# Kernel tuning notes

Measured on AMD Instinct MI355X. Metric: run time of the kernel, lower is better.

Reference implementation:

```python
import jax, jax.numpy as jnp
import numpy as np

B, S, D, H = 2, 2048, 1024, 16
DK = D // H

def setup_inputs() -> dict:
    key = jax.random.key(0)
    ks = jax.random.split(key, 12)
    def lin(k, shape, fan_in):
        bound = 1.0 / np.sqrt(fan_in)
        return jax.random.uniform(k, shape, jnp.float32, -bound, bound)
    inp = {
        'Q': jax.random.normal(ks[0], (B, S, D), jnp.float32),
        'K': jax.random.normal(ks[1], (B, S, D), jnp.float32),
        'V': jax.random.normal(ks[2], (B, S, D), jnp.float32),
        # padding mask: last 128 key positions of batch element 0 are padding
        'padding_mask': jnp.ones((B, 1, 1, S), jnp.int32).at[0, :, :, -128:].set(0),
        # causal look-ahead mask
        'look_ahead_mask': jnp.tril(jnp.ones((S, S), jnp.int32))[None, None],
        'Wq': lin(ks[3], (D, D), D), 'bq': lin(ks[4], (D,), D),
        'Wk': lin(ks[5], (D, D), D), 'bk': lin(ks[6], (D,), D),
        'Wv': lin(ks[7], (D, D), D), 'bv': lin(ks[8], (D,), D),
        'Wo': lin(ks[9], (D, D), D), 'bo': lin(ks[10], (D,), D),
    }
    return inp

def _split_heads(x):
    # [B,S,D] -> [B,H,S,DK]
    b, s, _ = x.shape
    return x.reshape(b, s, H, DK).transpose(0, 2, 1, 3)

def reference(Q, K, V, padding_mask, look_ahead_mask, Wq, bq, Wk, bk, Wv, bv, Wo, bo):
    q = _split_heads(Q @ Wq.T + bq)  # [B,H,S,DK]
    k = _split_heads(K @ Wk.T + bk)
    v = _split_heads(V @ Wv.T + bv)
    scores = jnp.einsum('bhqd,bhkd->bhqk', q, k) / np.sqrt(DK).astype(np.float32)
    neg_inf = jnp.float32(-jnp.inf)
    scores = jnp.where(padding_mask == 0, neg_inf, scores)
    scores = jnp.where(look_ahead_mask == 0, neg_inf, scores)
    weights = jax.nn.softmax(scores, axis=-1)  # dropout is identity in eval mode
    x = jnp.einsum('bhqk,bhkd->bhqd', weights, v)  # [B,H,S,DK]
    x = x.transpose(0, 2, 1, 3).reshape(Q.shape[0], Q.shape[1], D)
    return x @ Wo.T + bo
```

## Files before the change

### kernel.cpp

```cpp
#include <hip/hip_runtime.h>
#include <hip/hip_bf16.h>

#define B_   2
#define S_   2048
#define D_   1024
#define H_   16
#define DK_  64

typedef unsigned short u16;
typedef __attribute__((ext_vector_type(8))) short bf16x8;
typedef __attribute__((ext_vector_type(4))) float f32x4;

static __device__ __forceinline__ u16 f2bf(float f) {
  union { float f; unsigned u; } v; v.f = f;
  unsigned r = v.u + 0x7FFF + ((v.u >> 16) & 1);
  return (u16)(r >> 16);
}

static __device__ __forceinline__ void gl_lds16(const void* g, void* l) {
  __builtin_amdgcn_global_load_lds(
      (const __attribute__((address_space(1))) void*)g,
      (__attribute__((address_space(3))) void*)l, 16, 0, 0);
}

__global__ void cvt3(const float4* __restrict__ a, const float4* __restrict__ b, const float4* __restrict__ c,
                     ushort4* __restrict__ oa, ushort4* __restrict__ ob, ushort4* __restrict__ oc, int n4) {
  int y = blockIdx.y;
  const float4* in = (y == 0) ? a : (y == 1) ? b : c;
  ushort4* out = (y == 0) ? oa : (y == 1) ? ob : oc;
  int i = blockIdx.x * blockDim.x + threadIdx.x;
  if (i < n4) {
    float4 v = in[i];
    ushort4 r;
    r.x = f2bf(v.x); r.y = f2bf(v.y); r.z = f2bf(v.z); r.w = f2bf(v.w);
    out[i] = r;
  }
}
__global__ void cvt4(const float4* __restrict__ a, const float4* __restrict__ b, const float4* __restrict__ c,
                     const float4* __restrict__ d, ushort4* __restrict__ oa, ushort4* __restrict__ ob,
                     ushort4* __restrict__ oc, ushort4* __restrict__ od, int n4) {
  int y = blockIdx.y;
  const float4* in = (y == 0) ? a : (y == 1) ? b : (y == 2) ? c : d;
  ushort4* out = (y == 0) ? oa : (y == 1) ? ob : (y == 2) ? oc : od;
  int i = blockIdx.x * blockDim.x + threadIdx.x;
  if (i < n4) {
    float4 v = in[i];
    ushort4 r;
    r.x = f2bf(v.x); r.y = f2bf(v.y); r.z = f2bf(v.z); r.w = f2bf(v.w);
    out[i] = r;
  }
}

__launch_bounds__(256, 2)
__global__ void gemm_qkv(const u16* __restrict__ Xq, const u16* __restrict__ Xk, const u16* __restrict__ Xv,
                         const u16* __restrict__ Wq, const u16* __restrict__ Wk, const u16* __restrict__ Wv,
                         const float* __restrict__ bq, const float* __restrict__ bk, const float* __restrict__ bv,
                         u16* __restrict__ outq, u16* __restrict__ outk, u16* __restrict__ outv) {
  const int z = blockIdx.z;
  const u16* Am; const u16* Bm; int m0, n0;
  if (z == 2) { Am = Wv; Bm = Xv; m0 = blockIdx.x * 128; n0 = blockIdx.y * 128; }
  else if (z == 1) { Am = Xk; Bm = Wk; m0 = blockIdx.y * 128; n0 = blockIdx.x * 128; }
  else { Am = Xq; Bm = Wq; m0 = blockIdx.y * 128; n0 = blockIdx.x * 128; }
  const float* bias = (z == 0) ? bq : (z == 1) ? bk : bv;

  __shared__ __align__(16) u16 As[128 * 32];
  __shared__ __align__(16) u16 Bs[128 * 32];

  const int tid = threadIdx.x, lane = tid & 63, w = tid >> 6;
  const int q = lane >> 4, cl = lane & 15;
  const int wr = w >> 1, wc = w & 1;

  f32x4 acc[4][4] = {};

  for (int k0 = 0; k0 < D_; k0 += 32) {
#pragma unroll
    for (int i = 0; i < 2; ++i) {
      int cb = (i * 4 + w) * 64;
      int ch = cb + lane;
      int row = ch >> 2, ko = (ch & 3) << 3;
      gl_lds16(Am + (size_t)(m0 + row) * D_ + k0 + ko, As + cb * 8);
      gl_lds16(Bm + (size_t)(n0 + row) * D_ + k0 + ko, Bs + cb * 8);
    }
    __syncthreads();

    bf16x8 af[4], bfr[4];
#pragma unroll
    for (int r = 0; r < 4; ++r) af[r]  = *(const bf16x8*)(As + (wr * 64 + r * 16 + cl) * 32 + q * 8);
#pragma unroll
    for (int c = 0; c < 4; ++c) bfr[c] = *(const bf16x8*)(Bs + (wc * 64 + c * 16 + cl) * 32 + q * 8);
#pragma unroll
    for (int r = 0; r < 4; ++r)
#pragma unroll
      for (int c = 0; c < 4; ++c)
        acc[r][c] = __builtin_amdgcn_mfma_f32_16x16x32_bf16(af[r], bfr[c], acc[r][c], 0, 0, 0);
    __syncthreads();
  }

  if (z == 2) {
#pragma unroll
    for (int r = 0; r < 4; ++r) {
#pragma unroll
      for (int rr = 0; rr < 4; ++rr) {
        int j = m0 + wr * 64 + r * 16 + q * 4 + rr;
        float bval = bias[j];
        int hh = j >> 6, dk = j & 63;
#pragma unroll
        for (int c = 0; c < 4; ++c) {
          int n = n0 + wc * 64 + c * 16 + cl;
          int bb = n >> 11, s = n & (S_ - 1);
          outv[((size_t)(bb * H_ + hh) * DK_ + dk) * S_ + s] = f2bf(acc[r][c][rr] + bval);
        }
      }
    }
  } else {
    const float scale = (z == 0) ? 0.125f : 1.0f;
    u16* o = (z == 0) ? outq : outk;
#pragma unroll
    for (int c = 0; c < 4; ++c) {
      int j = n0 + wc * 64 + c * 16 + cl;
      float bval = bias[j];
      int hh = j >> 6, dk = j & 63;
#pragma unroll
      for (int r = 0; r < 4; ++r) {
#pragma unroll
        for (int rr = 0; rr < 4; ++rr) {
          int n = m0 + wr * 64 + r * 16 + q * 4 + rr;
          int bb = n >> 11, s = n & (S_ - 1);
          o[((size_t)(bb * H_ + hh) * S_ + s) * DK_ + dk] = f2bf((acc[r][c][rr] + bval) * scale);
        }
      }
    }
  }
}

__launch_bounds__(256, 2)
__global__ void attn(const u16* __restrict__ qh, const u16* __restrict__ kh,
                     const u16* __restrict__ vt, const int* __restrict__ pad,
                     u16* __restrict__ attn_out) {
  __shared__ __align__(16) u16 Ks[64 * 64];
  __shared__ __align__(16) u16 Vs[64 * 64];
  __shared__ __align__(16) u16 Ps[4][16 * 72];
  __shared__ float Kbias[64];

  const int tid = threadIdx.x, lane = tid & 63, w = tid >> 6;
  const int q = lane >> 4, cl = lane & 15;
  const int qt = (int)gridDim.x - 1 - (int)blockIdx.x;
  const int qb = qt * 64, h = blockIdx.y, b = blockIdx.z;

  const u16* Q = qh + (size_t)(b * H_ + h) * S_ * DK_;
  const u16* K = kh + (size_t)(b * H_ + h) * S_ * DK_;
  const u16* V = vt + (size_t)(b * H_ + h) * DK_ * S_;
  const int* pm = pad + b * S_;

  const int qr0 = qb + w * 16;
  bf16x8 qf0 = *(const bf16x8*)(Q + (qr0 + cl) * DK_ + q * 8);
  bf16x8 qf1 = *(const bf16x8*)(Q + (qr0 + cl) * DK_ + 32 + q * 8);

  f32x4 o[4] = {};
  float ls[4] = {0.f, 0.f, 0.f, 0.f};
  u16* Pw = Ps[w];

  const int nkv = qt + 1;
  for (int it = 0; it < nkv; ++it) {
    const int kb = it << 6;
#pragma unroll
    for (int i = 0; i < 2; ++i) {
      int s = (i * 4 + w) * 64 + lane;
      int row = s >> 3;
      int c = (s & 7) ^ (row & 7);
      gl_lds16(K + (size_t)(kb + row) * DK_ + (c << 3), Ks + (size_t)s * 8);
      gl_lds16(V + (size_t)row * S_ + kb + (c << 3), Vs + (size_t)s * 8);
    }
    if (tid < 64) {
      Kbias[tid] = (pm[kb + tid] != 0) ? -6.0f : -3e38f;
    }
    __syncthreads();

    f32x4 sa[4];
#pragma unroll
    for (int ct = 0; ct < 4; ++ct) {
      int rk = ct * 16 + cl;
      int c0 = q ^ (rk & 7);
      bf16x8 kf0 = *(const bf16x8*)(Ks + rk * 64 + (c0 << 3));
      bf16x8 kf1 = *(const bf16x8*)(Ks + rk * 64 + ((c0 ^ 4) << 3));
      f32x4 zz = {};
      zz = __builtin_amdgcn_mfma_f32_16x16x32_bf16(qf0, kf0, zz, 0, 0, 0);
      zz = __builtin_amdgcn_mfma_f32_16x16x32_bf16(qf1, kf1, zz, 0, 0, 0);
      sa[ct] = zz;
    }

    if (it < qt) {
#pragma unroll
      for (int ct = 0; ct < 4; ++ct) {
        float kbv = Kbias[ct * 16 + cl];
#pragma unroll
        for (int rr = 0; rr < 4; ++rr) {
          float p = __expf(sa[ct][rr] + kbv);
          ls[rr] += p;
          Pw[(q * 4 + rr) * 72 + ct * 16 + cl] = f2bf(p);
        }
      }
    } else {
#pragma unroll
      for (int ct = 0; ct < 4; ++ct) {
        int kg = kb + ct * 16 + cl;
        float kbv = Kbias[ct * 16 + cl];
#pragma unroll
        for (int rr = 0; rr < 4; ++rr) {
          int qg = qr0 + q * 4 + rr;
          float p = (kg <= qg) ? __expf(sa[ct][rr] + kbv) : 0.f;
          ls[rr] += p;
          Pw[(q * 4 + rr) * 72 + ct * 16 + cl] = f2bf(p);
        }
      }
    }

    bf16x8 pf0 = *(const bf16x8*)(Pw + cl * 72 + q * 8);
    bf16x8 pf1 = *(const bf16x8*)(Pw + cl * 72 + 32 + q * 8);

#pragma unroll
    for (int ct = 0; ct < 4; ++ct) {
      int rv = ct * 16 + cl;
      int c0 = q ^ (rv & 7);
      bf16x8 vf0 = *(const bf16x8*)(Vs + rv * 64 + (c0 << 3));
      bf16x8 vf1 = *(const bf16x8*)(Vs + rv * 64 + ((c0 ^ 4) << 3));
      o[ct] = __builtin_amdgcn_mfma_f32_16x16x32_bf16(pf0, vf0, o[ct], 0, 0, 0);
      o[ct] = __builtin_amdgcn_mfma_f32_16x16x32_bf16(pf1, vf1, o[ct], 0, 0, 0);
    }
    __syncthreads();
  }

#pragma unroll
  for (int rr = 0; rr < 4; ++rr) {
    float l = ls[rr];
    l += __shfl_xor(l, 1, 64);
    l += __shfl_xor(l, 2, 64);
    l += __shfl_xor(l, 4, 64);
    l += __shfl_xor(l, 8, 64);
    float inv = 1.0f / l;
    int qg = qr0 + q * 4 + rr;
    size_t base = (size_t)(b * S_ + qg) * D_ + h * DK_;
#pragma unroll
    for (int ct = 0; ct < 4; ++ct)
      attn_out[base + ct * 16 + cl] = f2bf(o[ct][rr] * inv);
  }
}

__launch_bounds__(256, 2)
__global__ void gemm_out(const u16* __restrict__ A, const u16* __restrict__ W,
                         const float* __restrict__ bias, float* __restrict__ out) {
  __shared__ __align__(16) u16 As[128 * 32];
  __shared__ __align__(16) u16 Bs[128 * 32];

  const int tid = threadIdx.x, lane = tid & 63, w = tid >> 6;
  const int q = lane >> 4, cl = lane & 15;
  const int wr = w >> 1, wc = w & 1;
  const int m0 = blockIdx.y * 128, n0 = blockIdx.x * 128;

  f32x4 acc[4][4] = {};

  for (int k0 = 0; k0 < D_; k0 += 32) {
#pragma unroll
    for (int i = 0; i < 2; ++i) {
      int cb = (i * 4 + w) * 64;
      int ch = cb + lane;
      int row = ch >> 2, ko = (ch & 3) << 3;
      gl_lds16(A + (size_t)(m0 + row) * D_ + k0 + ko, As + cb * 8);
      gl_lds16(W + (size_t)(n0 + row) * D_ + k0 + ko, Bs + cb * 8);
    }
    __syncthreads();

    bf16x8 af[4], bfr[4];
#pragma unroll
    for (int r = 0; r < 4; ++r) af[r]  = *(const bf16x8*)(As + (wr * 64 + r * 16 + cl) * 32 + q * 8);
#pragma unroll
    for (int c = 0; c < 4; ++c) bfr[c] = *(const bf16x8*)(Bs + (wc * 64 + c * 16 + cl) * 32 + q * 8);
#pragma unroll
    for (int r = 0; r < 4; ++r)
#pragma unroll
      for (int c = 0; c < 4; ++c)
        acc[r][c] = __builtin_amdgcn_mfma_f32_16x16x32_bf16(af[r], bfr[c], acc[r][c], 0, 0, 0);
    __syncthreads();
  }

#pragma unroll
  for (int c = 0; c < 4; ++c) {
    int j = n0 + wc * 64 + c * 16 + cl;
    float bval = bias[j];
#pragma unroll
    for (int r = 0; r < 4; ++r) {
#pragma unroll
      for (int rr = 0; rr < 4; ++rr) {
        int n = m0 + wr * 64 + r * 16 + q * 4 + rr;
        out[(size_t)n * D_ + j] = acc[r][c][rr] + bval;
      }
    }
  }
}

extern "C" void kernel_launch(void* const* d_in, const int* in_sizes, int n_in,
                              void* d_out, int out_size, void* d_ws, size_t ws_size,
                              hipStream_t stream) {
  const float* Qf  = (const float*)d_in[0];
  const float* Kf  = (const float*)d_in[1];
  const float* Vf  = (const float*)d_in[2];
  const int*   pad = (const int*)d_in[3];
  const float* Wqf = (const float*)d_in[5];
  const float* bq  = (const float*)d_in[6];
  const float* Wkf = (const float*)d_in[7];
  const float* bk  = (const float*)d_in[8];
  const float* Wvf = (const float*)d_in[9];
  const float* bv  = (const float*)d_in[10];
  const float* Wof = (const float*)d_in[11];
  const float* bo  = (const float*)d_in[12];

  const size_t BSD = (size_t)B_ * S_ * D_;
  const size_t DD  = (size_t)D_ * D_;

  char* ws = (char*)d_ws;
  u16* Qb   = (u16*)ws; ws += BSD * 2;
  u16* Kb   = (u16*)ws; ws += BSD * 2;
  u16* Vb   = (u16*)ws; ws += BSD * 2;
  u16* Wqb  = (u16*)ws; ws += DD * 2;
  u16* Wkb  = (u16*)ws; ws += DD * 2;
  u16* Wvb  = (u16*)ws; ws += DD * 2;
  u16* Wob  = (u16*)ws; ws += DD * 2;
  u16* qhd  = (u16*)ws; ws += BSD * 2;
  u16* khd  = (u16*)ws; ws += BSD * 2;
  u16* vtd  = (u16*)ws; ws += BSD * 2;
  u16* attn_o = (u16*)ws; ws += BSD * 2;

  const int n4 = (int)(BSD / 4);
  const int w4 = (int)(DD / 4);
  dim3 gc3(n4 / 256, 3), gc4(w4 / 256, 4);
  cvt3<<<gc3, 256, 0, stream>>>((const float4*)Qf, (const float4*)Kf, (const float4*)Vf,
                                (ushort4*)Qb, (ushort4*)Kb, (ushort4*)Vb, n4);
  cvt4<<<gc4, 256, 0, stream>>>((const float4*)Wqf, (const float4*)Wkf, (const float4*)Wvf, (const float4*)Wof,
                                (ushort4*)Wqb, (ushort4*)Wkb, (ushort4*)Wvb, (ushort4*)Wob, w4);

  dim3 g1(D_ / 128, (B_ * S_) / 128, 3);
  gemm_qkv<<<g1, 256, 0, stream>>>(Qb, Kb, Vb, Wqb, Wkb, Wvb, bq, bk, bv, qhd, khd, vtd);

  dim3 g2(S_ / 64, H_, B_);
  attn<<<g2, 256, 0, stream>>>(qhd, khd, vtd, pad, attn_o);

  dim3 g3(D_ / 128, (B_ * S_) / 128);
  gemm_out<<<g3, 256, 0, stream>>>(attn_o, Wob, bo, (float*)d_out);
}
```

Baseline: 257.2 us.

## Double-buffer K/V tiles and process 128 query rows per attention block

The attention kernel now handles 128 query rows per block (32 per wave, two MFMA row fragments), so each K/V tile loaded into LDS is reused across twice as many queries. K/V tiles are double-buffered: the next tile is prefetched while the current one is computed, which removes one barrier per iteration. The padding bias is read straight from global memory instead of through an LDS array. The query scale is folded to include log2(e) so exp2f replaces __expf, and the launch bound is raised to 3 blocks per SM. Register pressure rises and the grid shrinks by half, which may hurt occupancy or load balance across the causal triangle.

```diff
diff --git a/kernel.cpp b/kernel.cpp
--- a/kernel.cpp
+++ b/kernel.cpp
@@ -10,6 +10,9 @@
 typedef unsigned short u16;
 typedef __attribute__((ext_vector_type(8))) short bf16x8;
 typedef __attribute__((ext_vector_type(4))) float f32x4;
+
+#define QSCALE   0.18033688011112042f
+#define SMBIAS  -8.656170245333781f
 
 static __device__ __forceinline__ u16 f2bf(float f) {
   union { float f; unsigned u; } v; v.f = f;
@@ -113,7 +116,7 @@
       }
     }
   } else {
-    const float scale = (z == 0) ? 0.125f : 1.0f;
+    const float scale = (z == 0) ? QSCALE : 1.0f;
     u16* o = (z == 0) ? outq : outk;
 #pragma unroll
     for (int c = 0; c < 4; ++c) {
@@ -133,117 +136,158 @@
   }
 }
 
-__launch_bounds__(256, 2)
+__launch_bounds__(256, 3)
 __global__ void attn(const u16* __restrict__ qh, const u16* __restrict__ kh,
                      const u16* __restrict__ vt, const int* __restrict__ pad,
                      u16* __restrict__ attn_out) {
-  __shared__ __align__(16) u16 Ks[64 * 64];
-  __shared__ __align__(16) u16 Vs[64 * 64];
-  __shared__ __align__(16) u16 Ps[4][16 * 72];
-  __shared__ float Kbias[64];
+  __shared__ __align__(16) u16 Ks[2][64 * 64];
+  __shared__ __align__(16) u16 Vs[2][64 * 64];
+  __shared__ __align__(16) u16 Ps[4][32 * 72];
 
   const int tid = threadIdx.x, lane = tid & 63, w = tid >> 6;
   const int q = lane >> 4, cl = lane & 15;
   const int qt = (int)gridDim.x - 1 - (int)blockIdx.x;
-  const int qb = qt * 64, h = blockIdx.y, b = blockIdx.z;
+  const int qb = qt * 128, h = blockIdx.y, b = blockIdx.z;
 
   const u16* Q = qh + (size_t)(b * H_ + h) * S_ * DK_;
   const u16* K = kh + (size_t)(b * H_ + h) * S_ * DK_;
   const u16* V = vt + (size_t)(b * H_ + h) * DK_ * S_;
   const int* pm = pad + b * S_;
 
-  const int qr0 = qb + w * 16;
-  bf16x8 qf0 = *(const bf16x8*)(Q + (qr0 + cl) * DK_ + q * 8);
-  bf16x8 qf1 = *(const bf16x8*)(Q + (qr0 + cl) * DK_ + 32 + q * 8);
-
-  f32x4 o[4] = {};
-  float ls[4] = {0.f, 0.f, 0.f, 0.f};
+  const int qr0 = qb + w * 32;
+  bf16x8 qf[2][2];
+#pragma unroll
+  for (int f = 0; f < 2; ++f) {
+    qf[f][0] = *(const bf16x8*)(Q + (qr0 + f * 16 + cl) * DK_ + q * 8);
+    qf[f][1] = *(const bf16x8*)(Q + (qr0 + f * 16 + cl) * DK_ + 32 + q * 8);
+  }
+
+  f32x4 o[2][4] = {};
+  float ls[2][4] = {};
   u16* Pw = Ps[w];
 
-  const int nkv = qt + 1;
+  const int nkv = 2 * qt + 2;
+
+#pragma unroll
+  for (int i = 0; i < 2; ++i) {
+    int s = (i * 4 + w) * 64 + lane;
+    int row = s >> 3;
+    int c = (s & 7) ^ (row & 7);
+    gl_lds16(K + (size_t)row * DK_ + (c << 3), Ks[0] + (size_t)s * 8);
+    gl_lds16(V + (size_t)row * S_ + (c << 3), Vs[0] + (size_t)s * 8);
+  }
+
   for (int it = 0; it < nkv; ++it) {
     const int kb = it << 6;
-#pragma unroll
-    for (int i = 0; i < 2; ++i) {
-      int s = (i * 4 + w) * 64 + lane;
-      int row = s >> 3;
-      int c = (s & 7) ^ (row & 7);
-      gl_lds16(K + (size_t)(kb + row) * DK_ + (c << 3), Ks + (size_t)s * 8);
-      gl_lds16(V + (size_t)row * S_ + kb + (c << 3), Vs + (size_t)s * 8);
-    }
-    if (tid < 64) {
-      Kbias[tid] = (pm[kb + tid] != 0) ? -6.0f : -3e38f;
-    }
-    __syncthreads();
-
-    f32x4 sa[4];
+    const int buf = it & 1;
+    __syncthreads();
+
+    if (it + 1 < nkv) {
+      const int kb2 = (it + 1) << 6;
+#pragma unroll
+      for (int i = 0; i < 2; ++i) {
+        int s = (i * 4 + w) * 64 + lane;
+        int row = s >> 3;
+        int c = (s & 7) ^ (row & 7);
+        gl_lds16(K + (size_t)(kb2 + row) * DK_ + (c << 3), Ks[buf ^ 1] + (size_t)s * 8);
+        gl_lds16(V + (size_t)row * S_ + kb2 + (c << 3), Vs[buf ^ 1] + (size_t)s * 8);
+      }
+    }
+
+    if (kb > qr0 + 31) continue;
+
+    const u16* Kt = Ks[buf];
+    const u16* Vt = Vs[buf];
+
+    bf16x8 kf[4][2];
 #pragma unroll
     for (int ct = 0; ct < 4; ++ct) {
       int rk = ct * 16 + cl;
       int c0 = q ^ (rk & 7);
-      bf16x8 kf0 = *(const bf16x8*)(Ks + rk * 64 + (c0 << 3));
-      bf16x8 kf1 = *(const bf16x8*)(Ks + rk * 64 + ((c0 ^ 4) << 3));
-      f32x4 zz = {};
-      zz = __builtin_amdgcn_mfma_f32_16x16x32_bf16(qf0, kf0, zz, 0, 0, 0);
-      zz = __builtin_amdgcn_mfma_f32_16x16x32_bf16(qf1, kf1, zz, 0, 0, 0);
-      sa[ct] = zz;
-    }
-
-    if (it < qt) {
+      kf[ct][0] = *(const bf16x8*)(Kt + rk * 64 + (c0 << 3));
+      kf[ct][1] = *(const bf16x8*)(Kt + rk * 64 + ((c0 ^ 4) << 3));
+    }
+
+    float kbv[4];
+#pragma unroll
+    for (int ct = 0; ct < 4; ++ct)
+      kbv[ct] = (pm[kb + ct * 16 + cl] != 0) ? SMBIAS : -3e38f;
+
+    f32x4 sa[2][4];
+#pragma unroll
+    for (int f = 0; f < 2; ++f)
 #pragma unroll
       for (int ct = 0; ct < 4; ++ct) {
-        float kbv = Kbias[ct * 16 + cl];
-#pragma unroll
-        for (int rr = 0; rr < 4; ++rr) {
-          float p = __expf(sa[ct][rr] + kbv);
-          ls[rr] += p;
-          Pw[(q * 4 + rr) * 72 + ct * 16 + cl] = f2bf(p);
+        f32x4 zz = {};
+        zz = __builtin_amdgcn_mfma_f32_16x16x32_bf16(qf[f][0], kf[ct][0], zz, 0, 0, 0);
+        zz = __builtin_amdgcn_mfma_f32_16x16x32_bf16(qf[f][1], kf[ct][1], zz, 0, 0, 0);
+        sa[f][ct] = zz;
+      }
+
+    const bool needmask = (kb + 63 > qr0);
+    if (!needmask) {
+#pragma unroll
+      for (int f = 0; f < 2; ++f)
+#pragma unroll
+        for (int ct = 0; ct < 4; ++ct)
+#pragma unroll
+          for (int rr = 0; rr < 4; ++rr) {
+            float p = exp2f(sa[f][ct][rr] + kbv[ct]);
+            ls[f][rr] += p;
+            Pw[(f * 16 + q * 4 + rr) * 72 + ct * 16 + cl] = f2bf(p);
+          }
+    } else {
+#pragma unroll
+      for (int f = 0; f < 2; ++f)
+#pragma unroll
+        for (int ct = 0; ct < 4; ++ct) {
+          int kg = kb + ct * 16 + cl;
+#pragma unroll
+          for (int rr = 0; rr < 4; ++rr) {
+            int qg = qr0 + f * 16 + q * 4 + rr;
+            float p = (kg <= qg) ? exp2f(sa[f][ct][rr] + kbv[ct]) : 0.f;
+            ls[f][rr] += p;
+            Pw[(f * 16 + q * 4 + rr) * 72 + ct * 16 + cl] = f2bf(p);
+          }
         }
-      }
-    } else {
-#pragma unroll
-      for (int ct = 0; ct < 4; ++ct) {
-        int kg = kb + ct * 16 + cl;
-        float kbv = Kbias[ct * 16 + cl];
-#pragma unroll
-        for (int rr = 0; rr < 4; ++rr) {
-          int qg = qr0 + q * 4 + rr;
-          float p = (kg <= qg) ? __expf(sa[ct][rr] + kbv) : 0.f;
-          ls[rr] += p;
-          Pw[(q * 4 + rr) * 72 + ct * 16 + cl] = f2bf(p);
-        }
-      }
-    }
-
-    bf16x8 pf0 = *(const bf16x8*)(Pw + cl * 72 + q * 8);
-    bf16x8 pf1 = *(const bf16x8*)(Pw + cl * 72 + 32 + q * 8);
-
+    }
+
+    bf16x8 vf[4][2];
 #pragma unroll
     for (int ct = 0; ct < 4; ++ct) {
       int rv = ct * 16 + cl;
       int c0 = q ^ (rv & 7);
-      bf16x8 vf0 = *(const bf16x8*)(Vs + rv * 64 + (c0 << 3));
-      bf16x8 vf1 = *(const bf16x8*)(Vs + rv * 64 + ((c0 ^ 4) << 3));
-      o[ct] = __builtin_amdgcn_mfma_f32_16x16x32_bf16(pf0, vf0, o[ct], 0, 0, 0);
-      o[ct] = __builtin_amdgcn_mfma_f32_16x16x32_bf16(pf1, vf1, o[ct], 0, 0, 0);
-    }
-    __syncthreads();
-  }
-
-#pragma unroll
-  for (int rr = 0; rr < 4; ++rr) {
-    float l = ls[rr];
-    l += __shfl_xor(l, 1, 64);
-    l += __shfl_xor(l, 2, 64);
-    l += __shfl_xor(l, 4, 64);
-    l += __shfl_xor(l, 8, 64);
-    float inv = 1.0f / l;
-    int qg = qr0 + q * 4 + rr;
-    size_t base = (size_t)(b * S_ + qg) * D_ + h * DK_;
-#pragma unroll
-    for (int ct = 0; ct < 4; ++ct)
-      attn_out[base + ct * 16 + cl] = f2bf(o[ct][rr] * inv);
-  }
+      vf[ct][0] = *(const bf16x8*)(Vt + rv * 64 + (c0 << 3));
+      vf[ct][1] = *(const bf16x8*)(Vt + rv * 64 + ((c0 ^ 4) << 3));
+    }
+#pragma unroll
+    for (int f = 0; f < 2; ++f) {
+      bf16x8 pf0 = *(const bf16x8*)(Pw + (f * 16 + cl) * 72 + q * 8);
+      bf16x8 pf1 = *(const bf16x8*)(Pw + (f * 16 + cl) * 72 + 32 + q * 8);
+#pragma unroll
+      for (int ct = 0; ct < 4; ++ct) {
+        o[f][ct] = __builtin_amdgcn_mfma_f32_16x16x32_bf16(pf0, vf[ct][0], o[f][ct], 0, 0, 0);
+        o[f][ct] = __builtin_amdgcn_mfma_f32_16x16x32_bf16(pf1, vf[ct][1], o[f][ct], 0, 0, 0);
+      }
+    }
+  }
+
+#pragma unroll
+  for (int f = 0; f < 2; ++f)
+#pragma unroll
+    for (int rr = 0; rr < 4; ++rr) {
+      float l = ls[f][rr];
+      l += __shfl_xor(l, 1, 64);
+      l += __shfl_xor(l, 2, 64);
+      l += __shfl_xor(l, 4, 64);
+      l += __shfl_xor(l, 8, 64);
+      float inv = 1.0f / l;
+      int qg = qr0 + f * 16 + q * 4 + rr;
+      size_t base = (size_t)(b * S_ + qg) * D_ + h * DK_;
+#pragma unroll
+      for (int ct = 0; ct < 4; ++ct)
+        attn_out[base + ct * 16 + cl] = f2bf(o[f][ct][rr] * inv);
+    }
 }
 
 __launch_bounds__(256, 2)
@@ -341,7 +385,7 @@
   dim3 g1(D_ / 128, (B_ * S_) / 128, 3);
   gemm_qkv<<<g1, 256, 0, stream>>>(Qb, Kb, Vb, Wqb, Wkb, Wvb, bq, bk, bv, qhd, khd, vtd);
 
-  dim3 g2(S_ / 64, H_, B_);
+  dim3 g2(S_ / 128, H_, B_);
   attn<<<g2, 256, 0, stream>>>(qhd, khd, vtd, pad, attn_o);
 
   dim3 g3(D_ / 128, (B_ * S_) / 128);
```

Result: slower. 272.5 us (+5.9%).

## Double-buffer LDS tiles in GEMMs and attention, use exp2 softmax, retile output GEMM

Applied to the files above, without the earlier changes.

Adds two-stage LDS double buffering to the QKV GEMM, the attention loop and the output GEMM, so the next tile's global-to-LDS loads overlap compute and one barrier per iteration is removed. Attention folds log2(e) into the Q scale and bias so it can use exp2f, and it reads the padding mask directly per lane instead of staging it through LDS. The output GEMM moves to a 128x64 tile so twice as many blocks launch. The cost is higher LDS use, which may reduce occupancy, and a single barrier per iteration, which relies on correct ordering of the asynchronous LDS loads.

```diff
diff --git a/kernel.cpp b/kernel.cpp
--- a/kernel.cpp
+++ b/kernel.cpp
@@ -10,6 +10,9 @@
 typedef unsigned short u16;
 typedef __attribute__((ext_vector_type(8))) short bf16x8;
 typedef __attribute__((ext_vector_type(4))) float f32x4;
+
+#define QSCALE   0.18033688011112042f
+#define SMBIAS  -8.656170245333781f
 
 static __device__ __forceinline__ u16 f2bf(float f) {
   union { float f; unsigned u; } v; v.f = f;
@@ -63,37 +66,52 @@
   else { Am = Xq; Bm = Wq; m0 = blockIdx.y * 128; n0 = blockIdx.x * 128; }
   const float* bias = (z == 0) ? bq : (z == 1) ? bk : bv;
 
-  __shared__ __align__(16) u16 As[128 * 32];
-  __shared__ __align__(16) u16 Bs[128 * 32];
+  __shared__ __align__(16) u16 As[2][128 * 32];
+  __shared__ __align__(16) u16 Bs[2][128 * 32];
 
   const int tid = threadIdx.x, lane = tid & 63, w = tid >> 6;
   const int q = lane >> 4, cl = lane & 15;
   const int wr = w >> 1, wc = w & 1;
 
+#pragma unroll
+  for (int i = 0; i < 2; ++i) {
+    int cb = (i * 4 + w) * 64;
+    int ch = cb + lane;
+    int row = ch >> 2, ko = (ch & 3) << 3;
+    gl_lds16(Am + (size_t)(m0 + row) * D_ + ko, As[0] + cb * 8);
+    gl_lds16(Bm + (size_t)(n0 + row) * D_ + ko, Bs[0] + cb * 8);
+  }
+
   f32x4 acc[4][4] = {};
 
-  for (int k0 = 0; k0 < D_; k0 += 32) {
-#pragma unroll
-    for (int i = 0; i < 2; ++i) {
-      int cb = (i * 4 + w) * 64;
-      int ch = cb + lane;
-      int row = ch >> 2, ko = (ch & 3) << 3;
-      gl_lds16(Am + (size_t)(m0 + row) * D_ + k0 + ko, As + cb * 8);
-      gl_lds16(Bm + (size_t)(n0 + row) * D_ + k0 + ko, Bs + cb * 8);
-    }
+  for (int it = 0; it < 32; ++it) {
+    const int buf = it & 1;
     __syncthreads();
 
+    if (it < 31) {
+      const int k0 = (it + 1) * 32;
+#pragma unroll
+      for (int i = 0; i < 2; ++i) {
+        int cb = (i * 4 + w) * 64;
+        int ch = cb + lane;
+        int row = ch >> 2, ko = (ch & 3) << 3;
+        gl_lds16(Am + (size_t)(m0 + row) * D_ + k0 + ko, As[buf ^ 1] + cb * 8);
+        gl_lds16(Bm + (size_t)(n0 + row) * D_ + k0 + ko, Bs[buf ^ 1] + cb * 8);
+      }
+    }
+
+    const u16* At = As[buf];
+    const u16* Bt = Bs[buf];
     bf16x8 af[4], bfr[4];
 #pragma unroll
-    for (int r = 0; r < 4; ++r) af[r]  = *(const bf16x8*)(As + (wr * 64 + r * 16 + cl) * 32 + q * 8);
-#pragma unroll
-    for (int c = 0; c < 4; ++c) bfr[c] = *(const bf16x8*)(Bs + (wc * 64 + c * 16 + cl) * 32 + q * 8);
+    for (int r = 0; r < 4; ++r) af[r]  = *(const bf16x8*)(At + (wr * 64 + r * 16 + cl) * 32 + q * 8);
+#pragma unroll
+    for (int c = 0; c < 4; ++c) bfr[c] = *(const bf16x8*)(Bt + (wc * 64 + c * 16 + cl) * 32 + q * 8);
 #pragma unroll
     for (int r = 0; r < 4; ++r)
 #pragma unroll
       for (int c = 0; c < 4; ++c)
         acc[r][c] = __builtin_amdgcn_mfma_f32_16x16x32_bf16(af[r], bfr[c], acc[r][c], 0, 0, 0);
-    __syncthreads();
   }
 
   if (z == 2) {
@@ -113,7 +131,7 @@
       }
     }
   } else {
-    const float scale = (z == 0) ? 0.125f : 1.0f;
+    const float scale = (z == 0) ? QSCALE : 1.0f;
     u16* o = (z == 0) ? outq : outk;
 #pragma unroll
     for (int c = 0; c < 4; ++c) {
@@ -137,10 +155,9 @@
 __global__ void attn(const u16* __restrict__ qh, const u16* __restrict__ kh,
                      const u16* __restrict__ vt, const int* __restrict__ pad,
                      u16* __restrict__ attn_out) {
-  __shared__ __align__(16) u16 Ks[64 * 64];
-  __shared__ __align__(16) u16 Vs[64 * 64];
+  __shared__ __align__(16) u16 Ks[2][64 * 64];
+  __shared__ __align__(16) u16 Vs[2][64 * 64];
   __shared__ __align__(16) u16 Ps[4][16 * 72];
-  __shared__ float Kbias[64];
 
   const int tid = threadIdx.x, lane = tid & 63, w = tid >> 6;
   const int q = lane >> 4, cl = lane & 15;
@@ -161,54 +178,76 @@
   u16* Pw = Ps[w];
 
   const int nkv = qt + 1;
+
+#pragma unroll
+  for (int i = 0; i < 2; ++i) {
+    int s = (i * 4 + w) * 64 + lane;
+    int row = s >> 3;
+    int c = (s & 7) ^ (row & 7);
+    gl_lds16(K + (size_t)row * DK_ + (c << 3), Ks[0] + (size_t)s * 8);
+    gl_lds16(V + (size_t)row * S_ + (c << 3), Vs[0] + (size_t)s * 8);
+  }
+
   for (int it = 0; it < nkv; ++it) {
     const int kb = it << 6;
-#pragma unroll
-    for (int i = 0; i < 2; ++i) {
-      int s = (i * 4 + w) * 64 + lane;
-      int row = s >> 3;
-      int c = (s & 7) ^ (row & 7);
-      gl_lds16(K + (size_t)(kb + row) * DK_ + (c << 3), Ks + (size_t)s * 8);
-      gl_lds16(V + (size_t)row * S_ + kb + (c << 3), Vs + (size_t)s * 8);
-    }
-    if (tid < 64) {
-      Kbias[tid] = (pm[kb + tid] != 0) ? -6.0f : -3e38f;
-    }
+    const int buf = it & 1;
     __syncthreads();
 
-    f32x4 sa[4];
+    if (it + 1 < nkv) {
+      const int kb2 = (it + 1) << 6;
+#pragma unroll
+      for (int i = 0; i < 2; ++i) {
+        int s = (i * 4 + w) * 64 + lane;
+        int row = s >> 3;
+        int c = (s & 7) ^ (row & 7);
+        gl_lds16(K + (size_t)(kb2 + row) * DK_ + (c << 3), Ks[buf ^ 1] + (size_t)s * 8);
+        gl_lds16(V + (size_t)row * S_ + kb2 + (c << 3), Vs[buf ^ 1] + (size_t)s * 8);
+      }
+    }
+
+    const u16* Kt = Ks[buf];
+    const u16* Vt = Vs[buf];
+
+    bf16x8 kf[4][2];
 #pragma unroll
     for (int ct = 0; ct < 4; ++ct) {
       int rk = ct * 16 + cl;
       int c0 = q ^ (rk & 7);
-      bf16x8 kf0 = *(const bf16x8*)(Ks + rk * 64 + (c0 << 3));
-      bf16x8 kf1 = *(const bf16x8*)(Ks + rk * 64 + ((c0 ^ 4) << 3));
+      kf[ct][0] = *(const bf16x8*)(Kt + rk * 64 + (c0 << 3));
+      kf[ct][1] = *(const bf16x8*)(Kt + rk * 64 + ((c0 ^ 4) << 3));
+    }
+
+    float kbv[4];
+#pragma unroll
+    for (int ct = 0; ct < 4; ++ct)
+      kbv[ct] = (pm[kb + ct * 16 + cl] != 0) ? SMBIAS : -3e38f;
+
+    f32x4 sa[4];
+#pragma unroll
+    for (int ct = 0; ct < 4; ++ct) {
       f32x4 zz = {};
-      zz = __builtin_amdgcn_mfma_f32_16x16x32_bf16(qf0, kf0, zz, 0, 0, 0);
-      zz = __builtin_amdgcn_mfma_f32_16x16x32_bf16(qf1, kf1, zz, 0, 0, 0);
+      zz = __builtin_amdgcn_mfma_f32_16x16x32_bf16(qf0, kf[ct][0], zz, 0, 0, 0);
+      zz = __builtin_amdgcn_mfma_f32_16x16x32_bf16(qf1, kf[ct][1], zz, 0, 0, 0);
       sa[ct] = zz;
     }
 
     if (it < qt) {
 #pragma unroll
-      for (int ct = 0; ct < 4; ++ct) {
-        float kbv = Kbias[ct * 16 + cl];
+      for (int ct = 0; ct < 4; ++ct)
 #pragma unroll
         for (int rr = 0; rr < 4; ++rr) {
-          float p = __expf(sa[ct][rr] + kbv);
+          float p = exp2f(sa[ct][rr] + kbv[ct]);
           ls[rr] += p;
           Pw[(q * 4 + rr) * 72 + ct * 16 + cl] = f2bf(p);
         }
-      }
     } else {
 #pragma unroll
       for (int ct = 0; ct < 4; ++ct) {
         int kg = kb + ct * 16 + cl;
-        float kbv = Kbias[ct * 16 + cl];
 #pragma unroll
         for (int rr = 0; rr < 4; ++rr) {
           int qg = qr0 + q * 4 + rr;
-          float p = (kg <= qg) ? __expf(sa[ct][rr] + kbv) : 0.f;
+          float p = (kg <= qg) ? exp2f(sa[ct][rr] + kbv[ct]) : 0.f;
           ls[rr] += p;
           Pw[(q * 4 + rr) * 72 + ct * 16 + cl] = f2bf(p);
         }
@@ -222,12 +261,11 @@
     for (int ct = 0; ct < 4; ++ct) {
       int rv = ct * 16 + cl;
       int c0 = q ^ (rv & 7);
-      bf16x8 vf0 = *(const bf16x8*)(Vs + rv * 64 + (c0 << 3));
-      bf16x8 vf1 = *(const bf16x8*)(Vs + rv * 64 + ((c0 ^ 4) << 3));
+      bf16x8 vf0 = *(const bf16x8*)(Vt + rv * 64 + (c0 << 3));
+      bf16x8 vf1 = *(const bf16x8*)(Vt + rv * 64 + ((c0 ^ 4) << 3));
       o[ct] = __builtin_amdgcn_mfma_f32_16x16x32_bf16(pf0, vf0, o[ct], 0, 0, 0);
       o[ct] = __builtin_amdgcn_mfma_f32_16x16x32_bf16(pf1, vf1, o[ct], 0, 0, 0);
     }
-    __syncthreads();
   }
 
 #pragma unroll
@@ -249,49 +287,73 @@
 __launch_bounds__(256, 2)
 __global__ void gemm_out(const u16* __restrict__ A, const u16* __restrict__ W,
                          const float* __restrict__ bias, float* __restrict__ out) {
-  __shared__ __align__(16) u16 As[128 * 32];
-  __shared__ __align__(16) u16 Bs[128 * 32];
+  __shared__ __align__(16) u16 As[2][128 * 32];
+  __shared__ __align__(16) u16 Bs[2][64 * 32];
 
   const int tid = threadIdx.x, lane = tid & 63, w = tid >> 6;
   const int q = lane >> 4, cl = lane & 15;
-  const int wr = w >> 1, wc = w & 1;
-  const int m0 = blockIdx.y * 128, n0 = blockIdx.x * 128;
-
-  f32x4 acc[4][4] = {};
-
-  for (int k0 = 0; k0 < D_; k0 += 32) {
-#pragma unroll
-    for (int i = 0; i < 2; ++i) {
-      int cb = (i * 4 + w) * 64;
-      int ch = cb + lane;
-      int row = ch >> 2, ko = (ch & 3) << 3;
-      gl_lds16(A + (size_t)(m0 + row) * D_ + k0 + ko, As + cb * 8);
-      gl_lds16(W + (size_t)(n0 + row) * D_ + k0 + ko, Bs + cb * 8);
-    }
+  const int m0 = blockIdx.y * 128, n0 = blockIdx.x * 64;
+
+#pragma unroll
+  for (int i = 0; i < 2; ++i) {
+    int cb = (i * 4 + w) * 64;
+    int ch = cb + lane;
+    int row = ch >> 2, ko = (ch & 3) << 3;
+    gl_lds16(A + (size_t)(m0 + row) * D_ + ko, As[0] + cb * 8);
+  }
+  {
+    int cb = w * 64;
+    int ch = cb + lane;
+    int row = ch >> 2, ko = (ch & 3) << 3;
+    gl_lds16(W + (size_t)(n0 + row) * D_ + ko, Bs[0] + cb * 8);
+  }
+
+  f32x4 acc[2][4] = {};
+
+  for (int it = 0; it < 32; ++it) {
+    const int buf = it & 1;
     __syncthreads();
 
-    bf16x8 af[4], bfr[4];
-#pragma unroll
-    for (int r = 0; r < 4; ++r) af[r]  = *(const bf16x8*)(As + (wr * 64 + r * 16 + cl) * 32 + q * 8);
-#pragma unroll
-    for (int c = 0; c < 4; ++c) bfr[c] = *(const bf16x8*)(Bs + (wc * 64 + c * 16 + cl) * 32 + q * 8);
-#pragma unroll
-    for (int r = 0; r < 4; ++r)
+    if (it < 31) {
+      const int k0 = (it + 1) * 32;
+#pragma unroll
+      for (int i = 0; i < 2; ++i) {
+        int cb = (i * 4 + w) * 64;
+        int ch = cb + lane;
+        int row = ch >> 2, ko = (ch & 3) << 3;
+        gl_lds16(A + (size_t)(m0 + row) * D_ + k0 + ko, As[buf ^ 1] + cb * 8);
+      }
+      {
+        int cb = w * 64;
+        int ch = cb + lane;
+        int row = ch >> 2, ko = (ch & 3) << 3;
+        gl_lds16(W + (size_t)(n0 + row) * D_ + k0 + ko, Bs[buf ^ 1] + cb * 8);
+      }
+    }
+
+    const u16* At = As[buf];
+    const u16* Bt = Bs[buf];
+    bf16x8 af[2], bfr[4];
+#pragma unroll
+    for (int r = 0; r < 2; ++r) af[r]  = *(const bf16x8*)(At + (w * 32 + r * 16 + cl) * 32 + q * 8);
+#pragma unroll
+    for (int c = 0; c < 4; ++c) bfr[c] = *(const bf16x8*)(Bt + (c * 16 + cl) * 32 + q * 8);
+#pragma unroll
+    for (int r = 0; r < 2; ++r)
 #pragma unroll
       for (int c = 0; c < 4; ++c)
         acc[r][c] = __builtin_amdgcn_mfma_f32_16x16x32_bf16(af[r], bfr[c], acc[r][c], 0, 0, 0);
-    __syncthreads();
   }
 
 #pragma unroll
   for (int c = 0; c < 4; ++c) {
-    int j = n0 + wc * 64 + c * 16 + cl;
+    int j = n0 + c * 16 + cl;
     float bval = bias[j];
 #pragma unroll
-    for (int r = 0; r < 4; ++r) {
+    for (int r = 0; r < 2; ++r) {
 #pragma unroll
       for (int rr = 0; rr < 4; ++rr) {
-        int n = m0 + wr * 64 + r * 16 + q * 4 + rr;
+        int n = m0 + w * 32 + r * 16 + q * 4 + rr;
         out[(size_t)n * D_ + j] = acc[r][c][rr] + bval;
       }
     }
@@ -344,6 +406,6 @@
   dim3 g2(S_ / 64, H_, B_);
   attn<<<g2, 256, 0, stream>>>(qhd, khd, vtd, pad, attn_o);
 
-  dim3 g3(D_ / 128, (B_ * S_) / 128);
+  dim3 g3(D_ / 64, (B_ * S_) / 128);
   gemm_out<<<g3, 256, 0, stream>>>(attn_o, Wob, bo, (float*)d_out);
 }
```

After: 288.6 us. 1.12x slower.
